# Kernel tuning notes

Measured on AMD Instinct MI355X. Metric: run time of the kernel, lower is better.

Reference implementation:

```python
import jax, jax.numpy as jnp
import numpy as np

EPS = 2e-5
NCG = 51  # int(64 / 1.25)

def _conv1d(x, w, d):
    # x: [B,C,L], w: [Co,Ci,K]; dilated 1D conv, SAME padding
    return jax.lax.conv_general_dilated(x, w, window_strides=(1,), padding='SAME',
                                        rhs_dilation=(d,), dimension_numbers=('NCH', 'OIH', 'NCH'))

def _lift(x, w, n_h=9):
    # GConvRdG: lift R1 -> R1xR+; scale h=2^s realized as kernel dilation, 1/h normalization
    return jnp.stack([_conv1d(x, w, 2 ** s) / (2.0 ** s) for s in range(n_h)], axis=2)

def _gg(x, w):
    # GConvGG on [B,C,H,L]; w: [Co,Ci,Nk,K]; h_crop: H_out = H - Nk + 1.
    # Output scale s mixes input scales s..s+Nk-1, each with spatial dilation 2^(s+i).
    Nk, H = w.shape[2], x.shape[2]
    outs = []
    for s in range(H - Nk + 1):
        acc = None
        for i in range(Nk):
            d = 2 ** (s + i)
            t = _conv1d(x[:, :, s + i, :], w[:, :, i, :], d) / float(d)
            acc = t if acc is None else acc + t
        outs.append(acc)
    return jnp.stack(outs, axis=2)

def _bn(x, g, b):
    # training-mode BatchNorm2d over [B,C,H,L], per-channel stats
    m = jnp.mean(x, axis=(0, 2, 3), keepdims=True)
    v = jnp.var(x, axis=(0, 2, 3), keepdims=True)
    return (x - m) * jax.lax.rsqrt(v + EPS) * g[None, :, None, None] + b[None, :, None, None]

def _pool4(x):
    # max_pooling_R1: kernel 4 stride 4 over spatial axis
    B, C, H, L = x.shape
    return jnp.max(x.reshape(B, C, H, L // 4, 4), axis=-1)

def _forward(x, w1, w2, w3, w4, w5, w6, w7, w8, w9, w10, w11,
             g1, b1, g2, b2, g3, b3, g4, b4, g5, b5, g6, b6, g7, b7, g8, b8, g9, b9, g10, b10):
    r = jax.nn.relu
    out = _lift(x, w1)                      # [B,51,9,L]
    out = _pool4(out)
    out = r(_bn(out, g1, b1))
    out = _pool4(out)
    out = r(_bn(_gg(out, w2), g2, b2))      # H 9->7
    out = r(_bn(_gg(out, w3), g3, b3))
    out = _pool4(out)
    out = r(_bn(_gg(out, w4), g4, b4))      # 7->5
    out = r(_bn(_gg(out, w5), g5, b5))
    out = _pool4(out)
    out = r(_bn(_gg(out, w6), g6, b6))      # 5->3
    out = r(_bn(_gg(out, w7), g7, b7))
    out = r(_bn(_gg(out, w8), g8, b8))
    out = _pool4(out)
    out = r(_bn(_gg(out, w9), g9, b9))      # 3->1
    out = r(_bn(_gg(out, w10), g10, b10))
    out = jnp.mean(out, axis=-1, keepdims=True)   # global mean over space -> [B,408,1,1]
    out = _gg(out, w11)                     # 1x1 classifier -> [B,10,1,1]
    out = jnp.max(out, axis=-2)             # max over h axis -> [B,10,1]
    return out.reshape(out.shape[0], 10)

def setup_inputs():
    key = jax.random.key(0)
    ks = jax.random.split(key, 16)
    c = NCG
    def w(k, shape):
        fan_in = float(np.prod(shape[1:]))
        return jax.random.normal(k, shape, jnp.float32) * fan_in ** -0.5
    inp = {
        'x': jax.random.normal(ks[0], (8, 1, 32768), jnp.float32),
        'w1': w(ks[1], (c, 1, 79)),
        'w2': w(ks[2], (c, c, 3, 3)),
        'w3': w(ks[3], (c, c, 1, 3)),
        'w4': w(ks[4], (2 * c, c, 3, 3)),
        'w5': w(ks[5], (2 * c, 2 * c, 1, 3)),
        'w6': w(ks[6], (4 * c, 2 * c, 3, 3)),
        'w7': w(ks[7], (4 * c, 4 * c, 1, 3)),
        'w8': w(ks[8], (4 * c, 4 * c, 1, 3)),
        'w9': w(ks[9], (8 * c, 4 * c, 3, 3)),
        'w10': w(ks[10], (8 * c, 8 * c, 1, 3)),
        'w11': w(ks[11], (10, 8 * c, 1, 1)),
    }
    widths = [c, c, c, 2 * c, 2 * c, 4 * c, 4 * c, 4 * c, 8 * c, 8 * c]
    for i, cw in enumerate(widths, 1):
        inp['g%d' % i] = jnp.ones((cw,), jnp.float32)
        inp['b%d' % i] = jnp.zeros((cw,), jnp.float32)
    return inp

def reference(x, w1, w2, w3, w4, w5, w6, w7, w8, w9, w10, w11,
              g1, b1, g2, b2, g3, b3, g4, b4, g5, b5, g6, b6, g7, b7, g8, b8, g9, b9, g10, b10):
    return _forward(x, w1, w2, w3, w4, w5, w6, w7, w8, w9, w10, w11,
                    g1, b1, g2, b2, g3, b3, g4, b4, g5, b5, g6, b6, g7, b7, g8, b8, g9, b9, g10, b10)
```

## Files before the change

### kernel.cpp

```cpp
#include <hip/hip_runtime.h>
#include <hip/hip_bf16.h>

#define EPSBN 2e-5f

typedef __attribute__((ext_vector_type(8))) short short8v;
typedef __attribute__((ext_vector_type(4))) float f32x4;

__device__ inline unsigned short f2bf(float f) {
  unsigned u = __float_as_uint(f);
  unsigned r = (u + 0x7FFFu + ((u >> 16) & 1u)) >> 16;
  return (unsigned short)r;
}
__device__ inline float bf2f(unsigned short h) {
  return __uint_as_float(((unsigned)h) << 16);
}

template <int CTRL>
__device__ inline float dpp_radd(float v) {
  int r = __builtin_amdgcn_update_dpp(0, __float_as_int(v), CTRL, 0xf, 0xf,
                                      true);
  return v + __int_as_float(r);
}

constexpr int XPADL = 9984;
constexpr int XPADR = 14336;
constexpr int PROW = XPADL + 32768 + XPADR;

__global__ __launch_bounds__(256) void pad_pair_kernel(
    const float* __restrict__ x, unsigned* __restrict__ xpH,
    unsigned* __restrict__ xpL) {
  const int i = blockIdx.x * 256 + threadIdx.x;
  if (i >= PROW) return;
  const int sb = blockIdx.y;
  const int s = sb >> 3;
  const int b = sb & 7;
  const int d = 1 << s;
  const int pos0 = i - XPADL;
  const int pos1 = pos0 + d;
  float v0 = (pos0 >= 0 && pos0 < 32768) ? x[b * 32768 + pos0] : 0.f;
  float v1 = (pos1 >= 0 && pos1 < 32768) ? x[b * 32768 + pos1] : 0.f;
  unsigned u0 = __float_as_uint(v0);
  unsigned h0 = u0 >> 16;
  unsigned lo0 =
      __float_as_uint(v0 - __uint_as_float(u0 & 0xffff0000u)) >> 16;
  unsigned u1 = __float_as_uint(v1);
  unsigned h1 = u1 >> 16;
  unsigned lo1 =
      __float_as_uint(v1 - __uint_as_float(u1 & 0xffff0000u)) >> 16;
  size_t o = (size_t)sb * PROW + i;
  xpH[o] = h0 | (h1 << 16);
  xpL[o] = lo0 | (lo1 << 16);
}

__global__ __launch_bounds__(256) void pack_w1_kernel(
    const float* __restrict__ W, short* __restrict__ A) {
  int idx = blockIdx.x * 256 + threadIdx.x;
  if (idx >= 9 * 64 * 96) return;
  int s = idx / (64 * 96);
  int rem = idx - s * 64 * 96;
  int co = rem / 96;
  int k = rem - co * 96;
  float v = 0.f;
  if (co < 51 && k < 79)
    v = W[co * 79 + k] * __uint_as_float((unsigned)(127 - s) << 23);
  unsigned short hi = f2bf(v);
  unsigned short lo = f2bf(v - bf2f(hi));
  A[(size_t)s * 2 * 64 * 96 + co * 96 + k] = (short)hi;
  A[(size_t)s * 2 * 64 * 96 + 64 * 96 + co * 96 + k] = (short)lo;
}

__global__ __launch_bounds__(256) void lift_mfma_kernel(
    const unsigned* __restrict__ xpH, const unsigned* __restrict__ xpL,
    const short* __restrict__ Apk1, float* __restrict__ y1,
    float* __restrict__ part1) {
  constexpr int P = 104;
  const int bid = blockIdx.x;
  const int lc = (bid & 7) * 64 + (bid >> 3);
  const int s = blockIdx.y;
  const int b = blockIdx.z;
  const int d = 1 << s;
  const int l0 = lc * 64;
  const int tid = threadIdx.x;
  const int lane = tid & 63;
  const int quad = lane >> 4;
  const int n0 = lane & 15;
  const int wv = tid >> 6;
  const int coBase = wv * 16;

  __shared__ __align__(16) short Bh[64 * P];
  __shared__ __align__(16) short Bl[64 * P];
  __shared__ float sCh[2][64];

  const int nB = tid & 63;
  const int rowW = ((nB & 3) << 4) | (nB >> 2);
  const int swzW = (nB & 3) << 3;
  const int ogu = __builtin_amdgcn_readfirstlane(tid >> 6);
  const unsigned* xqH = xpH + (size_t)(s * 8 + b) * PROW + XPADL + l0;
  const unsigned* xqL = xpL + (size_t)(s * 8 + b) * PROW + XPADL + l0;

#pragma unroll
  for (int r = 0; r < 3; ++r) {
    const int kb = (ogu + 4 * r) * 8;
    const int base = (kb - 39) * d;
    uint4 ph, pl;
    ph.x = xqH[base + nB];
    ph.y = xqH[base + 2 * d + nB];
    ph.z = xqH[base + 4 * d + nB];
    ph.w = xqH[base + 6 * d + nB];
    pl.x = xqL[base + nB];
    pl.y = xqL[base + 2 * d + nB];
    pl.z = xqL[base + 4 * d + nB];
    pl.w = xqL[base + 6 * d + nB];
    *(uint4*)(Bh + rowW * P + (kb ^ swzW)) = ph;
    *(uint4*)(Bl + rowW * P + (kb ^ swzW)) = pl;
  }

  const short* ApkS = Apk1 + (size_t)s * 2 * 64 * 96;
  const short* arowH = ApkS + (coBase + n0) * 96;
  const short* arowL = arowH + 64 * 96;

  __syncthreads();

  f32x4 acc[4];
#pragma unroll
  for (int t = 0; t < 4; ++t) acc[t] = (f32x4){0.f, 0.f, 0.f, 0.f};

#pragma unroll
  for (int ks = 0; ks < 3; ++ks) {
    short8v ah = *(const short8v*)(arowH + ks * 32 + quad * 8);
    short8v al = *(const short8v*)(arowL + ks * 32 + quad * 8);
#pragma unroll
    for (int t = 0; t < 4; ++t) {
      const int n = n0 + 16 * t;
      const int off = (ks * 32 + quad * 8) ^ (t << 3);
      short8v bh = *(const short8v*)(Bh + n * P + off);
      short8v bl = *(const short8v*)(Bl + n * P + off);
      acc[t] = __builtin_amdgcn_mfma_f32_16x16x32_bf16(ah, bh, acc[t], 0, 0, 0);
      acc[t] = __builtin_amdgcn_mfma_f32_16x16x32_bf16(ah, bl, acc[t], 0, 0, 0);
      acc[t] = __builtin_amdgcn_mfma_f32_16x16x32_bf16(al, bh, acc[t], 0, 0, 0);
    }
  }

#pragma unroll
  for (int reg = 0; reg < 4; ++reg) {
    const int co = coBase + quad * 4 + reg;
    float po = fmaxf(fmaxf(acc[0][reg], acc[1][reg]),
                     fmaxf(acc[2][reg], acc[3][reg]));
    const bool valid = (co < 51);
    if (valid) {
      y1[(((size_t)b * 51 + co) * 9 + s) * 8192 + (l0 >> 2) + n0] = po;
    }
    float us = valid ? po : 0.f;
    float sq = us * us;
    us = dpp_radd<0x128>(us);
    sq = dpp_radd<0x128>(sq);
    us = dpp_radd<0x124>(us);
    sq = dpp_radd<0x124>(sq);
    us = dpp_radd<0x122>(us);
    sq = dpp_radd<0x122>(sq);
    us = dpp_radd<0x121>(us);
    sq = dpp_radd<0x121>(sq);
    if (n0 == 0) {
      sCh[0][co] = us;
      sCh[1][co] = sq;
    }
  }
  __syncthreads();
  if (tid < 51) {
    float* pp = part1 + (size_t)lc * 128;
    atomicAdd(&pp[tid], sCh[0][tid]);
    atomicAdd(&pp[64 + tid], sCh[1][tid]);
  }
}

__global__ __launch_bounds__(128) void reduce_stats1_kernel(
    const float* __restrict__ p, float* __restrict__ st) {
  const int t = threadIdx.x;
  if (t >= 102) return;
  const int k0 = blockIdx.x * 64;
  const int off = (t < 51) ? t : (64 + t - 51);
  float s = 0.f;
  for (int k = k0; k < k0 + 64; ++k) s += p[k * 128 + off];
  atomicAdd(&st[(t < 51) ? t : (512 + t - 51)], s);
}

__global__ __launch_bounds__(256) void stats_kernel(
    const float* __restrict__ Y, float* __restrict__ st, int C, int HL,
    int NS) {
  const int c = blockIdx.x, b = blockIdx.y, z = blockIdx.z;
  const int slice = HL / NS;
  const float* p = Y + ((size_t)b * C + c) * HL + (size_t)z * slice;
  float s = 0.f, q = 0.f;
  for (int i = threadIdx.x; i < slice; i += 256) {
    float v = p[i];
    s += v;
    q += v * v;
  }
#pragma unroll
  for (int off = 32; off > 0; off >>= 1) {
    s += __shfl_down(s, off, 64);
    q += __shfl_down(q, off, 64);
  }
  __shared__ float ls[4], lq[4];
  const int wid = threadIdx.x >> 6, lane = threadIdx.x & 63;
  if (lane == 0) { ls[wid] = s; lq[wid] = q; }
  __syncthreads();
  if (threadIdx.x == 0) {
    atomicAdd(&st[c], ls[0] + ls[1] + ls[2] + ls[3]);
    atomicAdd(&st[512 + c], lq[0] + lq[1] + lq[2] + lq[3]);
  }
}

__global__ __launch_bounds__(256) void reduce_parts_kernel(
    const float* __restrict__ p, float* __restrict__ y, int n, int stride,
    int ns) {
  int i = blockIdx.x * 256 + threadIdx.x;
  if (i >= n) return;
  float s = 0.f;
  for (int k = 0; k < ns; ++k) s += p[(size_t)k * stride + i];
  y[i] = s;
}

__device__ inline void parts_bn(const float* __restrict__ pp, unsigned c,
                                float invN, const float* __restrict__ g,
                                const float* __restrict__ bb, float& sc,
                                float& bi) {
  float ssum = 0.f, sqs = 0.f;
#pragma unroll
  for (int k = 0; k < 8; ++k) {
    ssum += pp[k * 1024 + c];
    sqs += pp[k * 1024 + 512 + c];
  }
  float m = ssum * invN;
  float v = sqs * invN - m * m;
  sc = g[c] * rsqrtf(v + EPSBN);
  bi = bb[c] - m * sc;
}

__global__ __launch_bounds__(256) void bnrelu_pool_parts_kernel(
    const float* __restrict__ Y, const float* __restrict__ pp,
    const float* __restrict__ g, const float* __restrict__ bb,
    float* __restrict__ Z, int C, int H, int Lin, float invN,
    unsigned int total) {
  unsigned int idx = blockIdx.x * 256u + threadIdx.x;
  if (idx >= total) return;
  const unsigned int Lo = (unsigned int)(Lin >> 2);
  unsigned int lo = idx % Lo;
  unsigned int r1 = idx / Lo;
  unsigned int h = r1 % (unsigned int)H;
  unsigned int r2 = r1 / (unsigned int)H;
  unsigned int c = r2 % (unsigned int)C;
  unsigned int b = r2 / (unsigned int)C;
  float sc, bi;
  parts_bn(pp, c, invN, g, bb, sc, bi);
  const float* p = Y + (((size_t)b * C + c) * H + h) * Lin + 4u * lo;
  float a0 = p[0] * sc + bi, a1 = p[1] * sc + bi;
  float a2 = p[2] * sc + bi, a3 = p[3] * sc + bi;
  float r = fmaxf(fmaxf(a0, a1), fmaxf(a2, a3));
  Z[idx] = fmaxf(r, 0.f);
}

__global__ __launch_bounds__(256) void bnrelu_pool_bf16_parts_kernel(
    const float* __restrict__ Y, const float* __restrict__ pp,
    const float* __restrict__ g, const float* __restrict__ bb,
    unsigned short* __restrict__ Z, int C, int H, int Lin, float invN,
    unsigned int total) {
  unsigned int idx = blockIdx.x * 256u + threadIdx.x;
  if (idx >= total) return;
  const unsigned int Lo = (unsigned int)(Lin >> 2);
  unsigned int lo = idx % Lo;
  unsigned int r1 = idx / Lo;
  unsigned int h = r1 % (unsigned int)H;
  unsigned int r2 = r1 / (unsigned int)H;
  unsigned int c = r2 % (unsigned int)C;
  unsigned int b = r2 / (unsigned int)C;
  float sc, bi;
  parts_bn(pp, c, invN, g, bb, sc, bi);
  const float* p = Y + (((size_t)b * C + c) * H + h) * Lin + 4u * lo;
  float a0 = p[0] * sc + bi, a1 = p[1] * sc + bi;
  float a2 = p[2] * sc + bi, a3 = p[3] * sc + bi;
  float r = fmaxf(fmaxf(a0, a1), fmaxf(a2, a3));
  Z[idx] = f2bf(fmaxf(r, 0.f));
}

__global__ __launch_bounds__(256) void bnrelu_pool_bf16_pad_kernel(
    const float* __restrict__ Y, const float* __restrict__ st,
    const float* __restrict__ g, const float* __restrict__ bb,
    unsigned short* __restrict__ Z, int C, int H, int Lin, float invN,
    unsigned int total, int Lp, int PADL, unsigned int total2) {
  unsigned int idx = blockIdx.x * 256u + threadIdx.x;
  if (idx >= total2) return;
  const unsigned int Lo = (unsigned int)(Lin >> 2);
  if (idx >= total) {
    unsigned int hidx = idx - total;
    unsigned int r = hidx / (unsigned int)(2 * PADL);
    unsigned int o = hidx - r * (unsigned int)(2 * PADL);
    unsigned int pos = (o < (unsigned int)PADL) ? o : (Lo + o);
    Z[(size_t)r * Lp + pos] = 0;
    return;
  }
  unsigned int lo = idx % Lo;
  unsigned int r1 = idx / Lo;
  unsigned int h = r1 % (unsigned int)H;
  unsigned int r2 = r1 / (unsigned int)H;
  unsigned int c = r2 % (unsigned int)C;
  unsigned int b = r2 / (unsigned int)C;
  float m = st[c] * invN;
  float v = st[512 + c] * invN - m * m;
  float sc = g[c] * rsqrtf(v + EPSBN);
  float bi = bb[c] - m * sc;
  const float* p = Y + (((size_t)b * C + c) * H + h) * Lin + 4u * lo;
  float a0 = p[0] * sc + bi, a1 = p[1] * sc + bi;
  float a2 = p[2] * sc + bi, a3 = p[3] * sc + bi;
  float r = fmaxf(fmaxf(a0, a1), fmaxf(a2, a3));
  Z[(((size_t)b * C + c) * H + h) * Lp + PADL + lo] = f2bf(fmaxf(r, 0.f));
}

__global__ __launch_bounds__(256) void bnrelu_pool_bf16_parts_pad_kernel(
    const float* __restrict__ Y, const float* __restrict__ pp,
    const float* __restrict__ g, const float* __restrict__ bb,
    unsigned short* __restrict__ Z, int C, int H, int Lin, float invN,
    unsigned int total, int Lp, int PADL, unsigned int total2) {
  unsigned int idx = blockIdx.x * 256u + threadIdx.x;
  if (idx >= total2) return;
  const unsigned int Lo = (unsigned int)(Lin >> 2);
  if (idx >= total) {
    unsigned int hidx = idx - total;
    unsigned int r = hidx / (unsigned int)(2 * PADL);
    unsigned int o = hidx - r * (unsigned int)(2 * PADL);
    unsigned int pos = (o < (unsigned int)PADL) ? o : (Lo + o);
    Z[(size_t)r * Lp + pos] = 0;
    return;
  }
  unsigned int lo = idx % Lo;
  unsigned int r1 = idx / Lo;
  unsigned int h = r1 % (unsigned int)H;
  unsigned int r2 = r1 / (unsigned int)H;
  unsigned int c = r2 % (unsigned int)C;
  unsigned int b = r2 / (unsigned int)C;
  float sc, bi;
  parts_bn(pp, c, invN, g, bb, sc, bi);
  const float* p = Y + (((size_t)b * C + c) * H + h) * Lin + 4u * lo;
  float a0 = p[0] * sc + bi, a1 = p[1] * sc + bi;
  float a2 = p[2] * sc + bi, a3 = p[3] * sc + bi;
  float r = fmaxf(fmaxf(a0, a1), fmaxf(a2, a3));
  Z[(((size_t)b * C + c) * H + h) * Lp + PADL + lo] = f2bf(fmaxf(r, 0.f));
}

__global__ __launch_bounds__(256) void bnrelu_kernel(
    const float* __restrict__ Y, const float* __restrict__ st,
    const float* __restrict__ g, const float* __restrict__ bb,
    float* __restrict__ A, int C, int HL, float invN, unsigned int total) {
  unsigned int idx = blockIdx.x * 256u + threadIdx.x;
  if (idx >= total) return;
  unsigned int c = (idx / (unsigned int)HL) % (unsigned int)C;
  float m = st[c] * invN;
  float v = st[512 + c] * invN - m * m;
  float sc = g[c] * rsqrtf(v + EPSBN);
  float bi = bb[c] - m * sc;
  A[idx] = fmaxf(fmaf(Y[idx], sc, bi), 0.f);
}

__global__ __launch_bounds__(256) void bnrelu_bf16_parts_kernel(
    const float* __restrict__ Y, const float* __restrict__ pp,
    const float* __restrict__ g, const float* __restrict__ bb,
    unsigned short* __restrict__ A, int C, int HL, float invN,
    unsigned int total) {
  unsigned int idx = blockIdx.x * 256u + threadIdx.x;
  if (idx >= total) return;
  unsigned int c = (idx / (unsigned int)HL) % (unsigned int)C;
  float sc, bi;
  parts_bn(pp, c, invN, g, bb, sc, bi);
  A[idx] = f2bf(fmaxf(fmaf(Y[idx], sc, bi), 0.f));
}

__global__ __launch_bounds__(256) void pack_all_kernel(
    const float* __restrict__ w2, const float* __restrict__ w3,
    const float* __restrict__ w4, const float* __restrict__ w5,
    const float* __restrict__ w6, const float* __restrict__ w7,
    const float* __restrict__ w8, short* __restrict__ apk2) {
  int idx = blockIdx.x * 256 + threadIdx.x;
  const float* W;
  short* A;
  int Co, KTOT, KPAD, COPAD, nk3;
  int r = idx;
  if (r < 229376) {
    W = w2; A = apk2; Co = 51; KTOT = 459; KPAD = 512; COPAD = 64; nk3 = 9;
  } else if ((r -= 229376) < 86016) {
    W = w3; A = apk2 + 458752; Co = 51; KTOT = 153; KPAD = 192; COPAD = 64;
    nk3 = 3;
  } else if ((r -= 86016) < 327680) {
    W = w4; A = apk2 + 630784; Co = 102; KTOT = 459; KPAD = 512; COPAD = 128;
    nk3 = 9;
  } else if ((r -= 327680) < 204800) {
    W = w5; A = apk2 + 1286144; Co = 102; KTOT = 306; KPAD = 320; COPAD = 128;
    nk3 = 3;
  } else if ((r -= 204800) < 737280) {
    W = w6; A = apk2 + 1695744; Co = 204; KTOT = 918; KPAD = 960; COPAD = 256;
    nk3 = 9;
  } else if ((r -= 737280) < 491520) {
    W = w7; A = apk2 + 3170304; Co = 204; KTOT = 612; KPAD = 640; COPAD = 256;
    nk3 = 3;
  } else if ((r -= 491520) < 491520) {
    W = w8; A = apk2 + 4153344; Co = 204; KTOT = 612; KPAD = 640; COPAD = 256;
    nk3 = 3;
  } else {
    return;
  }
  const int CK = COPAD * KPAD;
  int s = r / CK;
  int rem = r - s * CK;
  int co = rem / KPAD;
  int kk = rem - co * KPAD;
  float v = 0.f;
  if (co < Co && kk < KTOT) {
    int i = (kk % nk3) / 3;
    float scale = __uint_as_float((unsigned)(127 - (s + i)) << 23);
    v = W[co * KTOT + kk] * scale;
  }
  unsigned short hi = f2bf(v);
  unsigned short lo = f2bf(v - bf2f(hi));
  A[(size_t)s * 2 * CK + co * KPAD + kk] = (short)hi;
  A[(size_t)s * 2 * CK + CK + co * KPAD + kk] = (short)lo;
}

template <int NKv, int LT, bool PADDED>
__global__ __launch_bounds__(256) void gg_mfma5_kernel(
    const unsigned short* __restrict__ X, const short* __restrict__ Apk,
    float* __restrict__ Y, float* __restrict__ part, int Ci, int Co, int Hin,
    int L, int nL, int KTOT, int KPAD, int COPAD, int Lp, int XP) {
  constexpr int T = LT / 16;
  constexpr int KO = 256 / LT;
  constexpr int RIT = 8 / KO;

  const int bx = blockIdx.x;
  const int lc = bx % nL;
  const int cog = bx / nL;
  const int s = blockIdx.y;
  const int b = blockIdx.z;
  const int Hout = Hin - NKv + 1;
  const int l0 = lc * LT;
  const int tid = threadIdx.x;
  const int lane = tid & 63;
  const int quad = lane >> 4;
  const int m0 = lane & 15;
  const int wv = tid >> 6;
  const int coBase = cog * 64 + wv * 16;

  __shared__ __align__(16) short Bh[LT * 72];
  __shared__ int roT[1024];
  __shared__ int shT[1024];
  __shared__ float sCh[2][64];

  for (int kk = tid; kk < KPAD; kk += 256) {
    int ro, sh;
    if (kk < KTOT) {
      int ci = kk / (3 * NKv);
      int rem = kk - ci * (3 * NKv);
      int i = rem / 3;
      int k = rem - 3 * i;
      ro = (ci * Hin + s + i) * Lp + XP;
      sh = (k - 1) * (1 << (s + i));
    } else {
      ro = PADDED ? XP : 0;
      sh = PADDED ? 0 : -(1 << 30);
    }
    roT[kk] = ro;
    shT[kk] = sh;
  }
  __syncthreads();

  f32x4 acc[T];
#pragma unroll
  for (int t = 0; t < T; ++t) acc[t] = (f32x4){0.f, 0.f, 0.f, 0.f};

  const short* ApkS = Apk + (size_t)s * 2 * COPAD * KPAD;
  const short* arowH = ApkS + (size_t)(coBase + m0) * KPAD;
  const short* arowL = arowH + (size_t)COPAD * KPAD;
  const unsigned short* Xb = X + (size_t)b * Ci * Hin * Lp;

  const int lB = tid & (LT - 1);
  const int oc0 = tid / LT;
  const int nch = (KTOT + 63) >> 6;

  uint4 v0[RIT], v1[RIT], v2[RIT];
  auto gather = [&](int c0, uint4 (&pk)[RIT]) {
#pragma unroll
    for (int r = 0; r < RIT; ++r) {
      const int oct = oc0 + KO * r;
      const int kkb = (c0 << 6) + oct * 8;
      unsigned w[8];
#pragma unroll
      for (int j = 0; j < 8; ++j) {
        const int kk = kkb + j;
        if (PADDED) {
          w[j] = (unsigned)Xb[roT[kk] + l0 + lB + shT[kk]];
        } else {
          const int pos = l0 + lB + shT[kk];
          const int posc = min(max(pos, 0), L - 1);
          unsigned u = (unsigned)Xb[roT[kk] + posc];
          w[j] = ((unsigned)pos < (unsigned)L) ? u : 0u;
        }
      }
      pk[r].x = w[0] | (w[1] << 16);
      pk[r].y = w[2] | (w[3] << 16);
      pk[r].z = w[4] | (w[5] << 16);
      pk[r].w = w[6] | (w[7] << 16);
    }
  };

  gather(0, v0);
  if (nch > 1) gather(1, v1);
  for (int c0 = 0; c0 < nch; ++c0) {
#pragma unroll
    for (int r = 0; r < RIT; ++r)
      *(uint4*)(Bh + lB * 72 + (oc0 + KO * r) * 8) = v0[r];
    if (c0 + 2 < nch) gather(c0 + 2, v2);
    const int a0 = (c0 << 6) + quad * 8;
    short8v ah0 = *(const short8v*)(arowH + a0);
    short8v al0 = *(const short8v*)(arowL + a0);
    short8v ah1 = *(const short8v*)(arowH + a0 + 32);
    short8v al1 = *(const short8v*)(arowL + a0 + 32);
    __syncthreads();
#pragma unroll
    for (int t = 0; t < T; ++t) {
      const int l = m0 + 16 * t;
      short8v b0 = *(const short8v*)(Bh + l * 72 + quad * 8);
      short8v b1 = *(const short8v*)(Bh + l * 72 + 32 + quad * 8);
      acc[t] = __builtin_amdgcn_mfma_f32_16x16x32_bf16(ah0, b0, acc[t], 0, 0, 0);
      acc[t] = __builtin_amdgcn_mfma_f32_16x16x32_bf16(al0, b0, acc[t], 0, 0, 0);
      acc[t] = __builtin_amdgcn_mfma_f32_16x16x32_bf16(ah1, b1, acc[t], 0, 0, 0);
      acc[t] = __builtin_amdgcn_mfma_f32_16x16x32_bf16(al1, b1, acc[t], 0, 0, 0);
    }
    __syncthreads();
#pragma unroll
    for (int r = 0; r < RIT; ++r) {
      v0[r] = v1[r];
      v1[r] = v2[r];
    }
  }

#pragma unroll
  for (int reg = 0; reg < 4; ++reg) {
    const int co = coBase + quad * 4 + reg;
    float ss = 0.f, sq = 0.f;
    if (co < Co) {
      float* yp = Y + (((size_t)b * Co + co) * Hout + s) * L + l0;
#pragma unroll
      for (int t = 0; t < T; ++t) {
        float v = acc[t][reg];
        yp[m0 + 16 * t] = v;
        ss += v;
        sq = fmaf(v, v, sq);
      }
    }
    ss = dpp_radd<0x128>(ss);
    sq = dpp_radd<0x128>(sq);
    ss = dpp_radd<0x124>(ss);
    sq = dpp_radd<0x124>(sq);
    ss = dpp_radd<0x122>(ss);
    sq = dpp_radd<0x122>(sq);
    ss = dpp_radd<0x121>(ss);
    sq = dpp_radd<0x121>(sq);
    if (m0 == 0) {
      sCh[0][wv * 16 + quad * 4 + reg] = ss;
      sCh[1][wv * 16 + quad * 4 + reg] = sq;
    }
  }
  __syncthreads();
  if (tid < 64) {
    const int co = cog * 64 + tid;
    if (co < Co) {
      float* pp = part + (size_t)(lc & 7) * 1024;
      atomicAdd(&pp[co], sCh[0][tid]);
      atomicAdd(&pp[512 + co], sCh[1][tid]);
    }
  }
}

template <int NK, int L, int COSUB, int UN>
__global__ __launch_bounds__(256) void gg_tail3_kernel(
    const float* __restrict__ X, const float* __restrict__ W,
    float* __restrict__ Y, int Ci, int Co, int Hin, int NSPLIT, int ciPer,
    int partStride) {
  const int l = threadIdx.x % L;
  const int cs = threadIdx.x / L;
  const int co = blockIdx.x * COSUB + cs;
  const int s = blockIdx.y / NSPLIT;
  const int seg = blockIdx.y % NSPLIT;
  const int b = blockIdx.z;
  const int Hout = Hin - NK + 1;
  const int ciBeg = seg * ciPer;
  const int ciEnd = min(Ci, ciBeg + ciPer);

  float acc[NK];
#pragma unroll
  for (int i = 0; i < NK; ++i) acc[i] = 0.f;

  const float* wbase = W + (size_t)co * Ci * NK * 3;
  const float* xbase = X + ((size_t)b * Ci * Hin + s) * L;

  int ci = ciBeg;
  for (; ci + UN <= ciEnd; ci += UN) {
    float xv[UN][NK][3];
#pragma unroll
    for (int u = 0; u < UN; ++u) {
      const float* xr = xbase + (size_t)(ci + u) * (Hin * L);
#pragma unroll
      for (int i = 0; i < NK; ++i) {
        const int d = 1 << (s + i);
        const float* row = xr + i * L;
        xv[u][i][0] = (l >= d) ? row[l - d] : 0.f;
        xv[u][i][1] = row[l];
        xv[u][i][2] = (l + d < L) ? row[l + d] : 0.f;
      }
    }
#pragma unroll
    for (int u = 0; u < UN; ++u) {
      const float* wp = wbase + (ci + u) * (NK * 3);
#pragma unroll
      for (int i = 0; i < NK; ++i)
        acc[i] = fmaf(wp[3 * i], xv[u][i][0],
                      fmaf(wp[3 * i + 1], xv[u][i][1],
                           fmaf(wp[3 * i + 2], xv[u][i][2], acc[i])));
    }
  }
  for (; ci < ciEnd; ++ci) {
    const float* xr = xbase + (size_t)ci * (Hin * L);
    const float* wp = wbase + ci * (NK * 3);
#pragma unroll
    for (int i = 0; i < NK; ++i) {
      const int d = 1 << (s + i);
      const float* row = xr + i * L;
      float xm = (l >= d) ? row[l - d] : 0.f;
      float xc = row[l];
      float xp = (l + d < L) ? row[l + d] : 0.f;
      acc[i] = fmaf(wp[3 * i], xm,
                    fmaf(wp[3 * i + 1], xc, fmaf(wp[3 * i + 2], xp, acc[i])));
    }
  }
  float out = 0.f;
#pragma unroll
  for (int i = 0; i < NK; ++i) {
    float invd = __uint_as_float((unsigned)(127 - (s + i)) << 23);
    out = fmaf(acc[i], invd, out);
  }
  Y[(size_t)seg * partStride + (((size_t)b * Co + co) * Hout + s) * L + l] =
      out;
}

__global__ __launch_bounds__(256) void final_kernel(
    const float* __restrict__ Y, const float* __restrict__ st,
    const float* __restrict__ g, const float* __restrict__ bb,
    const float* __restrict__ w11, float* __restrict__ out) {
  const int b = blockIdx.x;
  const int tid = threadIdx.x;
  __shared__ float tch[408];
  for (int c = tid; c < 408; c += 256) {
    float m = st[c] * (1.f / 256.f);
    float v = st[512 + c] * (1.f / 256.f) - m * m;
    float sc = g[c] * rsqrtf(v + EPSBN);
    float bi = bb[c] - m * sc;
    const float* p = Y + ((size_t)b * 408 + c) * 32;
    float ssum = 0.f;
#pragma unroll
    for (int l = 0; l < 32; ++l) ssum += fmaxf(p[l] * sc + bi, 0.f);
    tch[c] = ssum * (1.f / 32.f);
  }
  __syncthreads();
  if (tid < 10) {
    float ssum = 0.f;
    for (int c = 0; c < 408; ++c) ssum += w11[tid * 408 + c] * tch[c];
    out[b * 10 + tid] = ssum;
  }
}

extern "C" void kernel_launch(void* const* d_in, const int* in_sizes, int n_in,
                              void* d_out, int out_size, void* d_ws,
                              size_t ws_size, hipStream_t stream) {
  const float* x = (const float*)d_in[0];
  const float* w1 = (const float*)d_in[1];
  const float* w2 = (const float*)d_in[2];
  const float* w3 = (const float*)d_in[3];
  const float* w4 = (const float*)d_in[4];
  const float* w5 = (const float*)d_in[5];
  const float* w6 = (const float*)d_in[6];
  const float* w7 = (const float*)d_in[7];
  const float* w8 = (const float*)d_in[8];
  const float* w9 = (const float*)d_in[9];
  const float* w10 = (const float*)d_in[10];
  const float* w11 = (const float*)d_in[11];
  const float* gg[11];
  const float* bbv[11];
  for (int i = 1; i <= 10; ++i) {
    gg[i] = (const float*)d_in[12 + 2 * (i - 1)];
    bbv[i] = (const float*)d_in[12 + 2 * (i - 1) + 1];
  }

  float* ws = (float*)d_ws;
  const size_t AR0 = 0;
  const size_t AR1 = 30081024;
  const size_t STATS = 38900000;
  float* y1 = ws + AR0;
  short* apk1 = (short*)(ws + AR1 + 460800);
  unsigned* xpairH = (unsigned*)(ws + AR1 + 520000);
  unsigned* xpairL = (unsigned*)(ws + AR1 + 4630336);
  float* part1 = ws + AR1 + 8740672;
  unsigned short* z1b = (unsigned short*)(ws + AR1);
  unsigned short* a3b = (unsigned short*)(ws + AR1);
  unsigned short* z3b = (unsigned short*)(ws + AR1);
  unsigned short* a5b = (unsigned short*)(ws + AR1 + 1500000);
  unsigned short* z5b = (unsigned short*)(ws + AR1);
  unsigned short* a6b = (unsigned short*)(ws + AR1 + 522240);
  unsigned short* a7b = (unsigned short*)(ws + AR1 + 1148928);
  float* z8 = ws + AR1;
  float* a9 = ws + AR1 + 1775616;
  float* part9 = ws + AR1 + 1900000;
  float* part10 = ws + AR1 + 2400000;
  float* y2 = ws + AR0;
  float* y3 = ws + AR0 + 5849088;
  float* y4 = ws + AR0;
  float* y5 = ws + AR0 + 2088960;
  float* y6 = ws + AR0;
  float* y7 = ws + AR0 + 626688;
  float* y8 = ws + AR0 + 1253376;
  float* y9 = ws + AR0;
  float* y10 = ws + AR0 + 104448;
  short* apk2 = (short*)(ws + 12000000);
  float* st[11];
  for (int i = 1; i <= 10; ++i) st[i] = ws + STATS + (size_t)(i - 1) * 1024;
  float* partg = ws + STATS + 10240;
  float* part2 = partg;
  float* part3 = partg + 8192;
  float* part4 = partg + 2 * 8192;
  float* part5 = partg + 3 * 8192;
  float* part6 = partg + 4 * 8192;
  float* part7 = partg + 5 * 8192;
  float* part8 = partg + 6 * 8192;

  hipMemsetAsync((void*)(ws + STATS), 0, 10 * 1024 * sizeof(float), stream);
  hipMemsetAsync((void*)part1, 0, 512 * 128 * sizeof(float), stream);
  hipMemsetAsync((void*)partg, 0, 7 * 8192 * sizeof(float), stream);

  pad_pair_kernel<<<dim3((PROW + 255) / 256, 72), 256, 0, stream>>>(
      x, xpairH, xpairL);
  pack_w1_kernel<<<(9 * 64 * 96 + 255) / 256, 256, 0, stream>>>(w1, apk1);
  lift_mfma_kernel<<<dim3(512, 9, 8), 256, 0, stream>>>(xpairH, xpairL, apk1,
                                                        y1, part1);
  reduce_stats1_kernel<<<8, 128, 0, stream>>>(part1, st[1]);
  {
    unsigned int tot = 8u * 51 * 9 * 2048;
    unsigned int tot2 = tot + 8u * 51 * 9 * 512;
    bnrelu_pool_bf16_pad_kernel<<<(tot2 + 255) / 256, 256, 0, stream>>>(
        y1, st[1], gg[1], bbv[1], z1b, 51, 9, 8192, 1.f / 589824.f, tot, 2560,
        256, tot2);
  }
  pack_all_kernel<<<(2568192 + 255) / 256, 256, 0, stream>>>(
      w2, w3, w4, w5, w6, w7, w8, apk2);
  gg_mfma5_kernel<3, 64, true><<<dim3(32, 7, 8), 256, 0, stream>>>(
      z1b, apk2, y2, part2, 51, 51, 9, 2048, 32, 459, 512, 64, 2560, 256);
  {
    unsigned int tot = 8u * 51 * 7 * 2048;
    bnrelu_bf16_parts_kernel<<<(tot + 255) / 256, 256, 0, stream>>>(
        y2, part2, gg[2], bbv[2], a3b, 51, 7 * 2048, 1.f / 114688.f, tot);
  }
  gg_mfma5_kernel<1, 64, false><<<dim3(32, 7, 8), 256, 0, stream>>>(
      a3b, apk2 + 458752, y3, part3, 51, 51, 7, 2048, 32, 153, 192, 64, 2048,
      0);
  {
    unsigned int tot = 8u * 51 * 7 * 512;
    bnrelu_pool_bf16_parts_kernel<<<(tot + 255) / 256, 256, 0, stream>>>(
        y3, part3, gg[3], bbv[3], z3b, 51, 7, 2048, 1.f / 114688.f, tot);
  }
  gg_mfma5_kernel<3, 32, false><<<dim3(32, 5, 8), 256, 0, stream>>>(
      z3b, apk2 + 630784, y4, part4, 51, 102, 7, 512, 16, 459, 512, 128, 512,
      0);
  {
    unsigned int tot = 8u * 102 * 5 * 512;
    bnrelu_bf16_parts_kernel<<<(tot + 255) / 256, 256, 0, stream>>>(
        y4, part4, gg[4], bbv[4], a5b, 102, 5 * 512, 1.f / 20480.f, tot);
  }
  gg_mfma5_kernel<1, 32, false><<<dim3(32, 5, 8), 256, 0, stream>>>(
      a5b, apk2 + 1286144, y5, part5, 102, 102, 5, 512, 16, 306, 320, 128,
      512, 0);
  {
    unsigned int tot = 8u * 102 * 5 * 128;
    unsigned int tot2 = tot + 8u * 102 * 5 * 32;
    bnrelu_pool_bf16_parts_pad_kernel<<<(tot2 + 255) / 256, 256, 0, stream>>>(
        y5, part5, gg[5], bbv[5], z5b, 102, 5, 512, 1.f / 20480.f, tot, 160,
        16, tot2);
  }
  gg_mfma5_kernel<3, 32, true><<<dim3(16, 3, 8), 256, 0, stream>>>(
      z5b, apk2 + 1695744, y6, part6, 102, 204, 5, 128, 4, 918, 960, 256, 160,
      16);
  {
    unsigned int tot = 8u * 204 * 3 * 128;
    bnrelu_bf16_parts_kernel<<<(tot + 255) / 256, 256, 0, stream>>>(
        y6, part6, gg[6], bbv[6], a6b, 204, 3 * 128, 1.f / 3072.f, tot);
  }
  gg_mfma5_kernel<1, 32, false><<<dim3(16, 3, 8), 256, 0, stream>>>(
      a6b, apk2 + 3170304, y7, part7, 204, 204, 3, 128, 4, 612, 640, 256, 128,
      0);
  {
    unsigned int tot = 8u * 204 * 3 * 128;
    bnrelu_bf16_parts_kernel<<<(tot + 255) / 256, 256, 0, stream>>>(
        y7, part7, gg[7], bbv[7], a7b, 204, 3 * 128, 1.f / 3072.f, tot);
  }
  gg_mfma5_kernel<1, 32, false><<<dim3(16, 3, 8), 256, 0, stream>>>(
      a7b, apk2 + 4153344, y8, part8, 204, 204, 3, 128, 4, 612, 640, 256, 128,
      0);
  {
    unsigned int tot = 8u * 204 * 3 * 32;
    bnrelu_pool_parts_kernel<<<(tot + 255) / 256, 256, 0, stream>>>(
        y8, part8, gg[8], bbv[8], z8, 204, 3, 128, 1.f / 3072.f, tot);
  }
  gg_tail3_kernel<3, 32, 8, 2><<<dim3(51, 4, 8), 256, 0, stream>>>(
      z8, w9, part9, 204, 408, 3, 4, 51, 104448);
  reduce_parts_kernel<<<(104448 + 255) / 256, 256, 0, stream>>>(
      part9, y9, 104448, 104448, 4);
  stats_kernel<<<dim3(408, 8, 1), 256, 0, stream>>>(y9, st[9], 408, 32, 1);
  {
    unsigned int tot = 8u * 408 * 32;
    bnrelu_kernel<<<(tot + 255) / 256, 256, 0, stream>>>(
        y9, st[9], gg[9], bbv[9], a9, 408, 32, 1.f / 256.f, tot);
  }
  gg_tail3_kernel<1, 32, 8, 8><<<dim3(51, 4, 8), 256, 0, stream>>>(
      a9, w10, part10, 408, 408, 1, 4, 102, 104448);
  reduce_parts_kernel<<<(104448 + 255) / 256, 256, 0, stream>>>(
      part10, y10, 104448, 104448, 4);
  stats_kernel<<<dim3(408, 8, 1), 256, 0, stream>>>(y10, st[10], 408, 32, 1);
  final_kernel<<<dim3(8), 256, 0, stream>>>(y10, st[10], gg[10], bbv[10], w11,
                                            (float*)d_out);
}
```

Baseline: 594.1 us.

## Fuse second max-pool into lift kernel by storing per-window max and min

The lift kernel now reduces each group of four pooled outputs across lanes with DPP, producing both a max and a min, and writes only these two quarter-size arrays instead of the full once-pooled tensor. The following BN+ReLU+pool kernel picks the max or the min according to the sign of the BN scale, which holds because an affine map with a negative scale reverses order. This cuts the intermediate y1 write and read from 8192 to two arrays of 2048 per row. The cost is extra DPP ops in the lift epilogue and a second output buffer.

```diff
diff --git a/kernel.cpp b/kernel.cpp
--- a/kernel.cpp
+++ b/kernel.cpp
@@ -20,6 +20,18 @@
   int r = __builtin_amdgcn_update_dpp(0, __float_as_int(v), CTRL, 0xf, 0xf,
                                       true);
   return v + __int_as_float(r);
+}
+template <int CTRL>
+__device__ inline float dpp_rmax(float v) {
+  int r = __builtin_amdgcn_update_dpp(0, __float_as_int(v), CTRL, 0xf, 0xf,
+                                      true);
+  return fmaxf(v, __int_as_float(r));
+}
+template <int CTRL>
+__device__ inline float dpp_rmin(float v) {
+  int r = __builtin_amdgcn_update_dpp(0, __float_as_int(v), CTRL, 0xf, 0xf,
+                                      true);
+  return fminf(v, __int_as_float(r));
 }
 
 constexpr int XPADL = 9984;
@@ -71,8 +83,8 @@
 
 __global__ __launch_bounds__(256) void lift_mfma_kernel(
     const unsigned* __restrict__ xpH, const unsigned* __restrict__ xpL,
-    const short* __restrict__ Apk1, float* __restrict__ y1,
-    float* __restrict__ part1) {
+    const short* __restrict__ Apk1, float* __restrict__ y1mx,
+    float* __restrict__ y1mn, float* __restrict__ part1) {
   constexpr int P = 104;
   const int bid = blockIdx.x;
   const int lc = (bid & 7) * 64 + (bid >> 3);
@@ -147,8 +159,14 @@
     float po = fmaxf(fmaxf(acc[0][reg], acc[1][reg]),
                      fmaxf(acc[2][reg], acc[3][reg]));
     const bool valid = (co < 51);
-    if (valid) {
-      y1[(((size_t)b * 51 + co) * 9 + s) * 8192 + (l0 >> 2) + n0] = po;
+    float mx = dpp_rmax<0xB1>(po);
+    mx = dpp_rmax<0x4E>(mx);
+    float mn = dpp_rmin<0xB1>(po);
+    mn = dpp_rmin<0x4E>(mn);
+    if (valid && (n0 & 3) == 0) {
+      size_t o = (((size_t)b * 51 + co) * 9 + s) * 2048 + (l0 >> 4) + (n0 >> 2);
+      y1mx[o] = mx;
+      y1mn[o] = mn;
     }
     float us = valid ? po : 0.f;
     float sq = us * us;
@@ -235,6 +253,35 @@
   float v = sqs * invN - m * m;
   sc = g[c] * rsqrtf(v + EPSBN);
   bi = bb[c] - m * sc;
+}
+
+__global__ __launch_bounds__(256) void bnrelu_minmax_pad_kernel(
+    const float* __restrict__ MX, const float* __restrict__ MN,
+    const float* __restrict__ st, const float* __restrict__ g,
+    const float* __restrict__ bb, unsigned short* __restrict__ Z, int C,
+    int H, int Lo, float invN, unsigned int total, int Lp, int PADL,
+    unsigned int total2) {
+  unsigned int idx = blockIdx.x * 256u + threadIdx.x;
+  if (idx >= total2) return;
+  if (idx >= total) {
+    unsigned int hidx = idx - total;
+    unsigned int r = hidx / (unsigned int)(2 * PADL);
+    unsigned int o = hidx - r * (unsigned int)(2 * PADL);
+    unsigned int pos = (o < (unsigned int)PADL) ? o : (Lo + o);
+    Z[(size_t)r * Lp + pos] = 0;
+    return;
+  }
+  unsigned int lo = idx % (unsigned int)Lo;
+  unsigned int r1 = idx / (unsigned int)Lo;
+  unsigned int r2 = r1 / (unsigned int)H;
+  unsigned int c = r2 % (unsigned int)C;
+  float m = st[c] * invN;
+  float v = st[512 + c] * invN - m * m;
+  float sc = g[c] * rsqrtf(v + EPSBN);
+  float bi = bb[c] - m * sc;
+  float a = (sc >= 0.f) ? MX[idx] : MN[idx];
+  float r = fmaxf(fmaf(a, sc, bi), 0.f);
+  Z[(size_t)r1 * Lp + PADL + lo] = f2bf(r);
 }
 
 __global__ __launch_bounds__(256) void bnrelu_pool_parts_kernel(
@@ -281,39 +328,6 @@
   float a2 = p[2] * sc + bi, a3 = p[3] * sc + bi;
   float r = fmaxf(fmaxf(a0, a1), fmaxf(a2, a3));
   Z[idx] = f2bf(fmaxf(r, 0.f));
-}
-
-__global__ __launch_bounds__(256) void bnrelu_pool_bf16_pad_kernel(
-    const float* __restrict__ Y, const float* __restrict__ st,
-    const float* __restrict__ g, const float* __restrict__ bb,
-    unsigned short* __restrict__ Z, int C, int H, int Lin, float invN,
-    unsigned int total, int Lp, int PADL, unsigned int total2) {
-  unsigned int idx = blockIdx.x * 256u + threadIdx.x;
-  if (idx >= total2) return;
-  const unsigned int Lo = (unsigned int)(Lin >> 2);
-  if (idx >= total) {
-    unsigned int hidx = idx - total;
-    unsigned int r = hidx / (unsigned int)(2 * PADL);
-    unsigned int o = hidx - r * (unsigned int)(2 * PADL);
-    unsigned int pos = (o < (unsigned int)PADL) ? o : (Lo + o);
-    Z[(size_t)r * Lp + pos] = 0;
-    return;
-  }
-  unsigned int lo = idx % Lo;
-  unsigned int r1 = idx / Lo;
-  unsigned int h = r1 % (unsigned int)H;
-  unsigned int r2 = r1 / (unsigned int)H;
-  unsigned int c = r2 % (unsigned int)C;
-  unsigned int b = r2 / (unsigned int)C;
-  float m = st[c] * invN;
-  float v = st[512 + c] * invN - m * m;
-  float sc = g[c] * rsqrtf(v + EPSBN);
-  float bi = bb[c] - m * sc;
-  const float* p = Y + (((size_t)b * C + c) * H + h) * Lin + 4u * lo;
-  float a0 = p[0] * sc + bi, a1 = p[1] * sc + bi;
-  float a2 = p[2] * sc + bi, a3 = p[3] * sc + bi;
-  float r = fmaxf(fmaxf(a0, a1), fmaxf(a2, a3));
-  Z[(((size_t)b * C + c) * H + h) * Lp + PADL + lo] = f2bf(fmaxf(r, 0.f));
 }
 
 __global__ __launch_bounds__(256) void bnrelu_pool_bf16_parts_pad_kernel(
@@ -701,7 +715,8 @@
   const size_t AR0 = 0;
   const size_t AR1 = 30081024;
   const size_t STATS = 38900000;
-  float* y1 = ws + AR0;
+  float* y1mx = ws + AR0;
+  float* y1mn = ws + AR0 + 7520256;
   short* apk1 = (short*)(ws + AR1 + 460800);
   unsigned* xpairH = (unsigned*)(ws + AR1 + 520000);
   unsigned* xpairL = (unsigned*)(ws + AR1 + 4630336);
@@ -746,14 +761,14 @@
       x, xpairH, xpairL);
   pack_w1_kernel<<<(9 * 64 * 96 + 255) / 256, 256, 0, stream>>>(w1, apk1);
   lift_mfma_kernel<<<dim3(512, 9, 8), 256, 0, stream>>>(xpairH, xpairL, apk1,
-                                                        y1, part1);
+                                                        y1mx, y1mn, part1);
   reduce_stats1_kernel<<<8, 128, 0, stream>>>(part1, st[1]);
   {
     unsigned int tot = 8u * 51 * 9 * 2048;
     unsigned int tot2 = tot + 8u * 51 * 9 * 512;
-    bnrelu_pool_bf16_pad_kernel<<<(tot2 + 255) / 256, 256, 0, stream>>>(
-        y1, st[1], gg[1], bbv[1], z1b, 51, 9, 8192, 1.f / 589824.f, tot, 2560,
-        256, tot2);
+    bnrelu_minmax_pad_kernel<<<(tot2 + 255) / 256, 256, 0, stream>>>(
+        y1mx, y1mn, st[1], gg[1], bbv[1], z1b, 51, 9, 2048, 1.f / 589824.f,
+        tot, 2560, 256, tot2);
   }
   pack_all_kernel<<<(2568192 + 255) / 256, 256, 0, stream>>>(
       w2, w3, w4, w5, w6, w7, w8, apk2);
```

After: 600.2 us. About the same (+1.0%).
